# Performance work log

Hardware: AMD Instinct MI355X
Metric: run time of the kernel (lower is better)

## Reference

```python
import jax, jax.numpy as jnp
import numpy as np

B, S_NEW, D = 2, 1024, 2048
CACHE_LEN = 4096
H, KVH, HD = 32, 8, 64
REP = H // KVH  # 4
POS = 3072


def setup_inputs() -> dict:
    key = jax.random.key(0)
    ks = jax.random.split(key, 11)
    sc = 0.02
    return {
        "x": jax.random.normal(ks[0], (B, S_NEW, D), jnp.float32),
        "k_cache": jax.random.normal(ks[1], (B, CACHE_LEN, KVH, HD), jnp.float32),
        "v_cache": jax.random.normal(ks[2], (B, CACHE_LEN, KVH, HD), jnp.float32),
        "Wq": jax.random.normal(ks[3], (D, H * HD), jnp.float32) * sc,
        "bq": jax.random.normal(ks[4], (H * HD,), jnp.float32) * sc,
        "Wk": jax.random.normal(ks[5], (D, KVH * HD), jnp.float32) * sc,
        "bk": jax.random.normal(ks[6], (KVH * HD,), jnp.float32) * sc,
        "Wv": jax.random.normal(ks[7], (D, KVH * HD), jnp.float32) * sc,
        "bv": jax.random.normal(ks[8], (KVH * HD,), jnp.float32) * sc,
        "Wo": jax.random.normal(ks[9], (H * HD, D), jnp.float32) * sc,
        "bo": jax.random.normal(ks[10], (D,), jnp.float32) * sc,
        "input_pos": POS,
    }


def reference(x, k_cache, v_cache, Wq, bq, Wk, bk, Wv, bv, Wo, bo, input_pos):
    b, s, _ = x.shape
    # projections
    q = (x @ Wq + bq).reshape(b, s, H, HD)
    k = (x @ Wk + bk).reshape(b, s, KVH, HD)
    v = (x @ Wv + bv).reshape(b, s, KVH, HD)
    # KV-cache append (input_pos is a static Python int)
    k_cache = jax.lax.dynamic_update_slice(k_cache, k, (0, input_pos, 0, 0))
    v_cache = jax.lax.dynamic_update_slice(v_cache, v, (0, input_pos, 0, 0))
    T = input_pos + s
    ck = k_cache[:b, :T]  # [b, T, KVH, HD]
    cv = v_cache[:b, :T]
    # GQA: query head h attends with kv head h // REP -> group q as [b, KVH, REP, s, HD]
    qg = q.reshape(b, s, KVH, REP, HD)
    scale = 1.0 / np.sqrt(HD).astype(np.float32)
    # scores: [b, KVH, REP, s, T]
    scores = jnp.einsum("bsgrd,btgd->bgrst", qg, ck) * scale
    weights = jax.nn.softmax(scores, axis=-1)
    # out: [b, KVH, REP, s, HD] -> [b, s, H*HD]
    z = jnp.einsum("bgrst,btgd->bsgrd", weights, cv).reshape(b, s, H * HD)
    return z @ Wo + bo
```

## Files before the change

### kernel.cpp

```cpp
#include <hip/hip_runtime.h>

#define BB   2
#define SS   1024
#define DD   2048
#define CL   4096
#define HH   32
#define KVH  8
#define HD   64
#define POS  3072
#define TTOT 4096
#define NQKV 3072

typedef __bf16 bfv8 __attribute__((ext_vector_type(8)));
typedef __bf16 bfv4 __attribute__((ext_vector_type(4)));
typedef unsigned short usv8 __attribute__((ext_vector_type(8)));
typedef unsigned short usv4 __attribute__((ext_vector_type(4)));
typedef float f32x4 __attribute__((ext_vector_type(4)));

#define QSCALE 0.18033688011112042f

static __device__ __forceinline__ unsigned short f2bf(float f) {
  return __builtin_bit_cast(unsigned short, (__bf16)f);
}

static __device__ __forceinline__ float fexp2(float x) {
  float r;
  asm("v_exp_f32 %0, %1" : "=v"(r) : "v"(x));
  return r;
}

static __device__ __forceinline__ f32x4 mfma16(bfv8 a, bfv8 b, f32x4 c) {
  return __builtin_amdgcn_mfma_f32_16x16x32_bf16(a, b, c, 0, 0, 0);
}

static __device__ __forceinline__ void gload16(const unsigned short* g, unsigned short* l) {
  typedef const __attribute__((address_space(1))) unsigned int GU;
  typedef __attribute__((address_space(3))) unsigned int LU;
  __builtin_amdgcn_global_load_lds((GU*)(unsigned long long)(uintptr_t)g,
                                   (LU*)(unsigned int)(uintptr_t)l, 16, 0, 0);
}

#define WAIT_VM0_BARRIER() do { \
  asm volatile("s_waitcnt vmcnt(0)" : : : "memory"); \
  __builtin_amdgcn_s_barrier(); } while (0)

__global__ __launch_bounds__(256) void conv_x_kernel(
    const float* __restrict__ x, const float* __restrict__ bq,
    const float* __restrict__ bk, const float* __restrict__ bv,
    unsigned short* __restrict__ xb, float* __restrict__ biasws) {
  int gid = blockIdx.x * 256 + threadIdx.x;
  if (gid < NQKV)
    biasws[gid] = gid < 2048 ? bq[gid] : (gid < 2560 ? bk[gid - 2048] : bv[gid - 2560]);
  f32x4 v = reinterpret_cast<const f32x4*>(x)[gid];
  usv4 o;
#pragma unroll
  for (int e = 0; e < 4; ++e) o[e] = f2bf(v[e]);
  reinterpret_cast<usv4*>(xb)[gid] = o;
}

__global__ __launch_bounds__(256) void trw_kernel(const float* __restrict__ src, int Ns,
                                                  unsigned short* __restrict__ dst) {
  __shared__ unsigned short L[64][72];
  const int n0 = blockIdx.x * 64, k0 = blockIdx.y * 64;
  const int tid = threadIdx.x;
#pragma unroll
  for (int p = 0; p < 4; ++p) {
    int r = p * 16 + (tid >> 4), c4 = tid & 15;
    f32x4 v = *reinterpret_cast<const f32x4*>(src + (long)(k0 + r) * Ns + n0 + c4 * 4);
#pragma unroll
    for (int e = 0; e < 4; ++e) L[r][c4 * 4 + e] = f2bf(v[e]);
  }
  __syncthreads();
  int n = tid >> 2, kc = (tid & 3) * 16;
  usv8 a, b;
#pragma unroll
  for (int e = 0; e < 8; ++e) { a[e] = L[kc + e][n]; b[e] = L[kc + 8 + e][n]; }
  unsigned short* dp = dst + (long)(n0 + n) * DD + k0 + kc;
  *reinterpret_cast<usv8*>(dp) = a;
  *reinterpret_cast<usv8*>(dp + 8) = b;
}

__global__ __launch_bounds__(256) void kcopy_kernel(const float* __restrict__ kc,
                                                    unsigned short* __restrict__ Kb) {
  int i = blockIdx.x * 256 + threadIdx.x;
  const int PERB = POS * KVH * 16;
  int b = i / PERB, rem = i - b * PERB;
  int t = rem / (KVH * 16), r2 = rem - t * (KVH * 16);
  int g = r2 >> 4, d4 = r2 & 15;
  f32x4 v = reinterpret_cast<const f32x4*>(kc)[(((long)((b * CL + t) * KVH + g)) << 4) + d4];
  usv4 o;
#pragma unroll
  for (int e = 0; e < 4; ++e) o[e] = f2bf(v[e]);
  reinterpret_cast<usv4*>(Kb)[(((long)((b * KVH + g) * CL + t)) << 4) + d4] = o;
}

__global__ __launch_bounds__(256) void vtrans_kernel(const float* __restrict__ vc,
                                                     unsigned short* __restrict__ Vb) {
  __shared__ unsigned short L[64][72];
  const int t0 = (blockIdx.x % 48) * 64;
  const int g = (blockIdx.x / 48) % KVH;
  const int b = blockIdx.x / (48 * KVH);
  const int tid = threadIdx.x;
  const int r = tid >> 2;
#pragma unroll
  for (int p = 0; p < 4; ++p) {
    int f = (tid & 3) + p * 4;
    f32x4 v = reinterpret_cast<const f32x4*>(vc)[(((long)(b * CL + t0 + r) * KVH + g) << 4) + f];
#pragma unroll
    for (int e = 0; e < 4; ++e) L[r][f * 4 + e] = f2bf(v[e]);
  }
  __syncthreads();
  int d = tid >> 2, tc = (tid & 3) * 16;
  usv8 a, b8;
#pragma unroll
  for (int e = 0; e < 8; ++e) { a[e] = L[tc + e][d]; b8[e] = L[tc + 8 + e][d]; }
  unsigned short* dp = Vb + (((long)((b * KVH + g) * HD + d)) << 12) + t0 + tc;
  *reinterpret_cast<usv8*>(dp) = a;
  *reinterpret_cast<usv8*>(dp + 8) = b8;
}

template <int MODE>
__global__ __launch_bounds__(256) void gemm2_kernel(
    const unsigned short* __restrict__ A, const unsigned short* __restrict__ Bt,
    const float* __restrict__ bias, float* __restrict__ outp,
    unsigned short* __restrict__ qout, unsigned short* __restrict__ kout,
    unsigned short* __restrict__ vout, int N, int K) {
  __shared__ unsigned short Al[2][64 * 32];
  __shared__ unsigned short Bl[2][128 * 32];
  const int tid = threadIdx.x;
  const int lane = tid & 63, w = tid >> 6;
  const int lr = lane & 15, lg = lane >> 4;
  const int wr = (w & 1) * 32, wc = (w >> 1) * 64;
  const int m0 = blockIdx.y * 64, n0 = blockIdx.x * 128;
  f32x4 acc[2][4];
#pragma unroll
  for (int a = 0; a < 2; ++a)
#pragma unroll
    for (int c = 0; c < 4; ++c) acc[a][c] = (f32x4){0.f, 0.f, 0.f, 0.f};

  const unsigned short* ga = A + (long)(m0 + 16 * w + (lane >> 2)) * K + (lane & 3) * 8;
  const unsigned short* gb = Bt + (long)(n0 + 32 * w + (lane >> 2)) * K + (lane & 3) * 8;
  unsigned short* const Al0 = &Al[0][0];
  unsigned short* const Al1 = &Al[1][0];
  unsigned short* const Bl0 = &Bl[0][0];
  unsigned short* const Bl1 = &Bl[1][0];
  const int wa = w * 512, wb = w * 1024;

  gload16(ga,          Al0 + wa);
  gload16(gb,          Bl0 + wb);
  gload16(gb + 16 * K, Bl0 + wb + 512);

  const int NIT = K >> 5;
  for (int it = 0; it < NIT; ++it) {
    WAIT_VM0_BARRIER();
    const bool odd = it & 1;
    const unsigned short* Ard = odd ? Al1 : Al0;
    const unsigned short* Brd = odd ? Bl1 : Bl0;
    if (it + 1 < NIT) {
      int kn = (it + 1) * 32;
      unsigned short* ad = (odd ? Al0 : Al1) + wa;
      unsigned short* bd = (odd ? Bl0 : Bl1) + wb;
      gload16(ga + kn,          ad);
      gload16(gb + kn,          bd);
      gload16(gb + kn + 16 * K, bd + 512);
    }
    bfv8 af[2], bf_[4];
#pragma unroll
    for (int mi = 0; mi < 2; ++mi)
      af[mi] = *reinterpret_cast<const bfv8*>(Ard + (wr + mi * 16 + lr) * 32 + lg * 8);
#pragma unroll
    for (int ni = 0; ni < 4; ++ni)
      bf_[ni] = *reinterpret_cast<const bfv8*>(Brd + (wc + ni * 16 + lr) * 32 + lg * 8);
#pragma unroll
    for (int mi = 0; mi < 2; ++mi)
#pragma unroll
      for (int ni = 0; ni < 4; ++ni)
        acc[mi][ni] = mfma16(af[mi], bf_[ni], acc[mi][ni]);
    __builtin_amdgcn_s_barrier();
  }

#pragma unroll
  for (int mi = 0; mi < 2; ++mi) {
#pragma unroll
    for (int ni = 0; ni < 4; ++ni) {
      int gn = n0 + wc + ni * 16 + lr;
      float bvl = bias[gn];
      float vals[4];
#pragma unroll
      for (int j = 0; j < 4; ++j) vals[j] = acc[mi][ni][j] + bvl;
      int gmb = m0 + wr + mi * 16 + lg * 4;
      if constexpr (MODE == 1) {
#pragma unroll
        for (int j = 0; j < 4; ++j) outp[(long)(gmb + j) * N + gn] = vals[j];
      } else {
        int b = gmb >> 10, s = gmb & 1023;
        if (gn < 2048) {
          int h = gn >> 6, d = gn & 63;
#pragma unroll
          for (int j = 0; j < 4; ++j)
            qout[(((long)((b * HH + h) * SS + s + j)) << 6) + d] = f2bf(vals[j] * QSCALE);
        } else if (gn < 2560) {
          int g = (gn - 2048) >> 6, d = gn & 63;
#pragma unroll
          for (int j = 0; j < 4; ++j)
            kout[(((long)((b * KVH + g) * CL + POS + s + j)) << 6) + d] = f2bf(vals[j]);
        } else {
          int g = (gn - 2560) >> 6, d = gn & 63;
          usv4 o;
#pragma unroll
          for (int j = 0; j < 4; ++j) o[j] = f2bf(vals[j]);
          *reinterpret_cast<usv4*>(vout + (((long)((b * KVH + g) * HD + d)) << 12) + POS + s) = o;
        }
      }
    }
  }
}

__global__ __launch_bounds__(256) void attn_kernel(
    const unsigned short* __restrict__ Q, const unsigned short* __restrict__ Kb,
    const unsigned short* __restrict__ Vb, unsigned short* __restrict__ Z) {
  __shared__ unsigned short Kl[2 * 64 * 64];
  __shared__ unsigned short Vl[2 * 64 * 64];
  __shared__ unsigned short Pl[4 * 16 * 64];

  const int tid = threadIdx.x;
  const int lane = tid & 63, w = tid >> 6;
  const int lr = lane & 15, lg = lane >> 4;
  const int s0 = blockIdx.x * 64;
  const int h = blockIdx.y, b = blockIdx.z, g = h >> 2;
  const int sw = s0 + w * 16;
  const int woff = w * 1024;

  const unsigned short* qb = Q + (((long)((b * HH + h) * SS + sw + lr)) << 6) + lg * 8;
  bfv8 qf0 = *reinterpret_cast<const bfv8*>(qb);
  bfv8 qf1 = *reinterpret_cast<const bfv8*>(qb + 32);

  const unsigned short* kg = Kb + (((long)(b * KVH + g)) << 18);
  const unsigned short* vg = Vb + (((long)(b * KVH + g)) << 18);

  const int rw = lane >> 3;
  const int ug = (lane & 7) ^ rw;
  const unsigned short* kA = kg + (16 * w + rw) * 64 + ug * 8;
  const unsigned short* vA = vg + (long)(16 * w + rw) * TTOT + ug * 8;

  unsigned short* const Kl0 = Kl;
  unsigned short* const Kl1 = Kl + 4096;
  unsigned short* const Vl0 = Vl;
  unsigned short* const Vl1 = Vl + 4096;

  const int sz = lr & 7;
  const int u0 = (lg ^ sz) * 8, u1 = ((lg ^ sz) ^ 4) * 8;

  const int swzP = (lr & 7) << 3;
  unsigned short* const prow = Pl + (w * 16 + lr) * 64;
  const int p0 = (lg * 8) ^ swzP, p1 = (32 + lg * 8) ^ swzP;

  f32x4 O[4];
#pragma unroll
  for (int dt = 0; dt < 4; ++dt) O[dt] = (f32x4){0.f, 0.f, 0.f, 0.f};
  float lsum = 0.f;

  gload16(kA,            Kl0 + woff);
  gload16(kA + 8 * 64,   Kl0 + woff + 512);
  gload16(vA,            Vl0 + woff);
  gload16(vA + 8 * TTOT, Vl0 + woff + 512);

  for (int it = 0; it < 64; ++it) {
    WAIT_VM0_BARRIER();
    const bool odd = it & 1;
    const unsigned short* krd = odd ? Kl1 : Kl0;
    const unsigned short* vrd = odd ? Vl1 : Vl0;
    if (it < 63) {
      int tn = (it + 1) * 64;
      unsigned short* kwd = (odd ? Kl0 : Kl1) + woff;
      unsigned short* vwd = (odd ? Vl0 : Vl1) + woff;
      gload16(kA + tn * 64,           kwd);
      gload16(kA + tn * 64 + 8 * 64,  kwd + 512);
      gload16(vA + tn,                vwd);
      gload16(vA + tn + 8 * TTOT,     vwd + 512);
    }

    __builtin_amdgcn_s_setprio(1);
    f32x4 sv[4];
#pragma unroll
    for (int tt = 0; tt < 4; ++tt) {
      const unsigned short* kr = krd + (tt * 16 + lr) * 64;
      bfv8 kf0 = *reinterpret_cast<const bfv8*>(kr + u0);
      bfv8 kf1 = *reinterpret_cast<const bfv8*>(kr + u1);
      f32x4 z = (f32x4){0.f, 0.f, 0.f, 0.f};
      z = mfma16(kf0, qf0, z);
      z = mfma16(kf1, qf1, z);
      sv[tt] = z;
    }
    __builtin_amdgcn_s_setprio(0);

    float ps = 0.f;
#pragma unroll
    for (int tt = 0; tt < 4; ++tt)
#pragma unroll
      for (int j = 0; j < 4; ++j) {
        float p = fexp2(sv[tt][j]);
        sv[tt][j] = p;
        ps += p;
      }
    lsum += ps;

#pragma unroll
    for (int tt = 0; tt < 4; ++tt) {
      bfv4 pv;
#pragma unroll
      for (int j = 0; j < 4; ++j) pv[j] = (__bf16)sv[tt][j];
      *reinterpret_cast<bfv4*>(&prow[(tt * 16 + lg * 4) ^ swzP]) = pv;
    }

    bfv8 pf0 = *reinterpret_cast<const bfv8*>(&prow[p0]);
    bfv8 pf1 = *reinterpret_cast<const bfv8*>(&prow[p1]);
    __builtin_amdgcn_s_setprio(1);
#pragma unroll
    for (int dt = 0; dt < 4; ++dt) {
      const unsigned short* vr = vrd + (dt * 16 + lr) * 64;
      bfv8 vf0 = *reinterpret_cast<const bfv8*>(vr + u0);
      bfv8 vf1 = *reinterpret_cast<const bfv8*>(vr + u1);
      O[dt] = mfma16(pf0, vf0, O[dt]);
      O[dt] = mfma16(pf1, vf1, O[dt]);
    }
    __builtin_amdgcn_s_setprio(0);
    __builtin_amdgcn_s_barrier();
  }

  lsum += __shfl_xor(lsum, 16);
  lsum += __shfl_xor(lsum, 32);
  float lj[4];
#pragma unroll
  for (int j = 0; j < 4; ++j) lj[j] = 1.0f / __shfl(lsum, lg * 4 + j);
#pragma unroll
  for (int dt = 0; dt < 4; ++dt)
#pragma unroll
    for (int j = 0; j < 4; ++j) {
      int s = sw + lg * 4 + j, d = dt * 16 + lr;
      Z[(((long)(b * SS + s)) << 11) + h * 64 + d] = f2bf(O[dt][j] * lj[j]);
    }
}

extern "C" void kernel_launch(void* const* d_in, const int* in_sizes, int n_in,
                              void* d_out, int out_size, void* d_ws, size_t ws_size,
                              hipStream_t stream) {
  const float* x  = (const float*)d_in[0];
  const float* kc = (const float*)d_in[1];
  const float* vc = (const float*)d_in[2];
  const float* Wq = (const float*)d_in[3];
  const float* bq = (const float*)d_in[4];
  const float* Wk = (const float*)d_in[5];
  const float* bk = (const float*)d_in[6];
  const float* Wv = (const float*)d_in[7];
  const float* bv = (const float*)d_in[8];
  const float* Wo = (const float*)d_in[9];
  const float* bo = (const float*)d_in[10];

  unsigned short* Kb    = (unsigned short*)d_ws;
  unsigned short* Vb    = Kb + 4194304;
  unsigned short* q_ws  = Vb + 4194304;
  unsigned short* xb    = q_ws + 4194304;
  unsigned short* z_ws  = xb;
  unsigned short* Wqkvt = xb + 4194304;
  unsigned short* Wot   = Wqkvt + 6291456;
  float* biasws = (float*)(Wot + 4194304);

  conv_x_kernel<<<4096, 256, 0, stream>>>(x, bq, bk, bv, xb, biasws);
  trw_kernel<<<dim3(32, 32), 256, 0, stream>>>(Wq, 2048, Wqkvt);
  trw_kernel<<<dim3(8, 32), 256, 0, stream>>>(Wk, 512, Wqkvt + (long)2048 * 2048);
  trw_kernel<<<dim3(8, 32), 256, 0, stream>>>(Wv, 512, Wqkvt + (long)2560 * 2048);
  trw_kernel<<<dim3(32, 32), 256, 0, stream>>>(Wo, 2048, Wot);
  kcopy_kernel<<<3072, 256, 0, stream>>>(kc, Kb);
  vtrans_kernel<<<768, 256, 0, stream>>>(vc, Vb);
  gemm2_kernel<0><<<dim3(24, 32), 256, 0, stream>>>(xb, Wqkvt, biasws, nullptr,
                                                    q_ws, Kb, Vb, NQKV, DD);
  attn_kernel<<<dim3(16, 32, 2), 256, 0, stream>>>(q_ws, Kb, Vb, z_ws);
  gemm2_kernel<1><<<dim3(16, 32), 256, 0, stream>>>(z_ws, Wot, bo, (float*)d_out,
                                                    nullptr, nullptr, nullptr, DD, DD);
}
```

Baseline: 321.2 us.

## Merge prep kernels, drop redundant loop barriers, split attention PV into halves

The four weight-transpose launches become one kernel, and the K-copy and V-transpose launches become another, with branching on block index. This cuts the number of small prep-kernel launches. The GEMM and attention main loops drop their trailing s_barrier, relying on the wait-plus-barrier at the top of each iteration to protect the double buffers. The GEMM MFMA block is also wrapped in setprio. In attention, the per-wave P staging buffer is halved and the PV product runs in two phases, so the second half's bf16 conversion and stores can overlap the first half's MFMAs. The cost is extra LDS round trips on a buffer that is reused within each iteration.

```diff
diff --git a/kernel.cpp b/kernel.cpp
--- a/kernel.cpp
+++ b/kernel.cpp
@@ -58,10 +58,19 @@
   reinterpret_cast<usv4*>(xb)[gid] = o;
 }
 
-__global__ __launch_bounds__(256) void trw_kernel(const float* __restrict__ src, int Ns,
-                                                  unsigned short* __restrict__ dst) {
+__global__ __launch_bounds__(256) void wtr_kernel(
+    const float* __restrict__ Wq, const float* __restrict__ Wk,
+    const float* __restrict__ Wv, const float* __restrict__ Wo,
+    unsigned short* __restrict__ Wqkvt, unsigned short* __restrict__ Wot) {
   __shared__ unsigned short L[64][72];
-  const int n0 = blockIdx.x * 64, k0 = blockIdx.y * 64;
+  const int bx = blockIdx.x, k0 = blockIdx.y * 64;
+  const float* src;
+  unsigned short* dst;
+  int Ns, n0;
+  if (bx < 32)      { src = Wq; Ns = 2048; dst = Wqkvt;                     n0 = bx * 64; }
+  else if (bx < 40) { src = Wk; Ns = 512;  dst = Wqkvt + (long)2048 * 2048; n0 = (bx - 32) * 64; }
+  else if (bx < 48) { src = Wv; Ns = 512;  dst = Wqkvt + (long)2560 * 2048; n0 = (bx - 40) * 64; }
+  else              { src = Wo; Ns = 2048; dst = Wot;                       n0 = (bx - 48) * 64; }
   const int tid = threadIdx.x;
 #pragma unroll
   for (int p = 0; p < 4; ++p) {
@@ -80,43 +89,44 @@
   *reinterpret_cast<usv8*>(dp + 8) = b;
 }
 
-__global__ __launch_bounds__(256) void kcopy_kernel(const float* __restrict__ kc,
-                                                    unsigned short* __restrict__ Kb) {
-  int i = blockIdx.x * 256 + threadIdx.x;
-  const int PERB = POS * KVH * 16;
-  int b = i / PERB, rem = i - b * PERB;
-  int t = rem / (KVH * 16), r2 = rem - t * (KVH * 16);
-  int g = r2 >> 4, d4 = r2 & 15;
-  f32x4 v = reinterpret_cast<const f32x4*>(kc)[(((long)((b * CL + t) * KVH + g)) << 4) + d4];
-  usv4 o;
-#pragma unroll
-  for (int e = 0; e < 4; ++e) o[e] = f2bf(v[e]);
-  reinterpret_cast<usv4*>(Kb)[(((long)((b * KVH + g) * CL + t)) << 4) + d4] = o;
-}
-
-__global__ __launch_bounds__(256) void vtrans_kernel(const float* __restrict__ vc,
-                                                     unsigned short* __restrict__ Vb) {
-  __shared__ unsigned short L[64][72];
-  const int t0 = (blockIdx.x % 48) * 64;
-  const int g = (blockIdx.x / 48) % KVH;
-  const int b = blockIdx.x / (48 * KVH);
+__global__ __launch_bounds__(256) void cache_kernel(
+    const float* __restrict__ kc, const float* __restrict__ vc,
+    unsigned short* __restrict__ Kb, unsigned short* __restrict__ Vb) {
   const int tid = threadIdx.x;
-  const int r = tid >> 2;
-#pragma unroll
-  for (int p = 0; p < 4; ++p) {
-    int f = (tid & 3) + p * 4;
-    f32x4 v = reinterpret_cast<const f32x4*>(vc)[(((long)(b * CL + t0 + r) * KVH + g) << 4) + f];
-#pragma unroll
-    for (int e = 0; e < 4; ++e) L[r][f * 4 + e] = f2bf(v[e]);
+  if (blockIdx.x < 3072) {
+    int i = blockIdx.x * 256 + tid;
+    const int PERB = POS * KVH * 16;
+    int b = i / PERB, rem = i - b * PERB;
+    int t = rem / (KVH * 16), r2 = rem - t * (KVH * 16);
+    int g = r2 >> 4, d4 = r2 & 15;
+    f32x4 v = reinterpret_cast<const f32x4*>(kc)[(((long)((b * CL + t) * KVH + g)) << 4) + d4];
+    usv4 o;
+#pragma unroll
+    for (int e = 0; e < 4; ++e) o[e] = f2bf(v[e]);
+    reinterpret_cast<usv4*>(Kb)[(((long)((b * KVH + g) * CL + t)) << 4) + d4] = o;
+  } else {
+    __shared__ unsigned short L[64][72];
+    const int bid = blockIdx.x - 3072;
+    const int t0 = (bid % 48) * 64;
+    const int g = (bid / 48) % KVH;
+    const int b = bid / (48 * KVH);
+    const int r = tid >> 2;
+#pragma unroll
+    for (int p = 0; p < 4; ++p) {
+      int f = (tid & 3) + p * 4;
+      f32x4 v = reinterpret_cast<const f32x4*>(vc)[(((long)(b * CL + t0 + r) * KVH + g) << 4) + f];
+#pragma unroll
+      for (int e = 0; e < 4; ++e) L[r][f * 4 + e] = f2bf(v[e]);
+    }
+    __syncthreads();
+    int d = tid >> 2, tc = (tid & 3) * 16;
+    usv8 a, b8;
+#pragma unroll
+    for (int e = 0; e < 8; ++e) { a[e] = L[tc + e][d]; b8[e] = L[tc + 8 + e][d]; }
+    unsigned short* dp = Vb + (((long)((b * KVH + g) * HD + d)) << 12) + t0 + tc;
+    *reinterpret_cast<usv8*>(dp) = a;
+    *reinterpret_cast<usv8*>(dp + 8) = b8;
   }
-  __syncthreads();
-  int d = tid >> 2, tc = (tid & 3) * 16;
-  usv8 a, b8;
-#pragma unroll
-  for (int e = 0; e < 8; ++e) { a[e] = L[tc + e][d]; b8[e] = L[tc + 8 + e][d]; }
-  unsigned short* dp = Vb + (((long)((b * KVH + g) * HD + d)) << 12) + t0 + tc;
-  *reinterpret_cast<usv8*>(dp) = a;
-  *reinterpret_cast<usv8*>(dp + 8) = b8;
 }
 
 template <int MODE>
@@ -171,12 +181,13 @@
 #pragma unroll
     for (int ni = 0; ni < 4; ++ni)
       bf_[ni] = *reinterpret_cast<const bfv8*>(Brd + (wc + ni * 16 + lr) * 32 + lg * 8);
+    __builtin_amdgcn_s_setprio(1);
 #pragma unroll
     for (int mi = 0; mi < 2; ++mi)
 #pragma unroll
       for (int ni = 0; ni < 4; ++ni)
         acc[mi][ni] = mfma16(af[mi], bf_[ni], acc[mi][ni]);
-    __builtin_amdgcn_s_barrier();
+    __builtin_amdgcn_s_setprio(0);
   }
 
 #pragma unroll
@@ -221,7 +232,7 @@
     const unsigned short* __restrict__ Vb, unsigned short* __restrict__ Z) {
   __shared__ unsigned short Kl[2 * 64 * 64];
   __shared__ unsigned short Vl[2 * 64 * 64];
-  __shared__ unsigned short Pl[4 * 16 * 64];
+  __shared__ unsigned short Pl[4 * 16 * 32];
 
   const int tid = threadIdx.x;
   const int lane = tid & 63, w = tid >> 6;
@@ -251,9 +262,9 @@
   const int sz = lr & 7;
   const int u0 = (lg ^ sz) * 8, u1 = ((lg ^ sz) ^ 4) * 8;
 
-  const int swzP = (lr & 7) << 3;
-  unsigned short* const prow = Pl + (w * 16 + lr) * 64;
-  const int p0 = (lg * 8) ^ swzP, p1 = (32 + lg * 8) ^ swzP;
+  const int swzP = (lr & 3) << 3;
+  unsigned short* const prow = Pl + (w * 16 + lr) * 32;
+  const int p0 = (lg * 8) ^ swzP;
 
   f32x4 O[4];
 #pragma unroll
@@ -306,26 +317,38 @@
     lsum += ps;
 
 #pragma unroll
-    for (int tt = 0; tt < 4; ++tt) {
+    for (int tt = 0; tt < 2; ++tt) {
       bfv4 pv;
 #pragma unroll
       for (int j = 0; j < 4; ++j) pv[j] = (__bf16)sv[tt][j];
       *reinterpret_cast<bfv4*>(&prow[(tt * 16 + lg * 4) ^ swzP]) = pv;
     }
-
     bfv8 pf0 = *reinterpret_cast<const bfv8*>(&prow[p0]);
-    bfv8 pf1 = *reinterpret_cast<const bfv8*>(&prow[p1]);
     __builtin_amdgcn_s_setprio(1);
 #pragma unroll
     for (int dt = 0; dt < 4; ++dt) {
       const unsigned short* vr = vrd + (dt * 16 + lr) * 64;
       bfv8 vf0 = *reinterpret_cast<const bfv8*>(vr + u0);
+      O[dt] = mfma16(pf0, vf0, O[dt]);
+    }
+    __builtin_amdgcn_s_setprio(0);
+
+#pragma unroll
+    for (int tt = 2; tt < 4; ++tt) {
+      bfv4 pv;
+#pragma unroll
+      for (int j = 0; j < 4; ++j) pv[j] = (__bf16)sv[tt][j];
+      *reinterpret_cast<bfv4*>(&prow[((tt - 2) * 16 + lg * 4) ^ swzP]) = pv;
+    }
+    bfv8 pf1 = *reinterpret_cast<const bfv8*>(&prow[p0]);
+    __builtin_amdgcn_s_setprio(1);
+#pragma unroll
+    for (int dt = 0; dt < 4; ++dt) {
+      const unsigned short* vr = vrd + (dt * 16 + lr) * 64;
       bfv8 vf1 = *reinterpret_cast<const bfv8*>(vr + u1);
-      O[dt] = mfma16(pf0, vf0, O[dt]);
       O[dt] = mfma16(pf1, vf1, O[dt]);
     }
     __builtin_amdgcn_s_setprio(0);
-    __builtin_amdgcn_s_barrier();
   }
 
   lsum += __shfl_xor(lsum, 16);
@@ -367,12 +390,8 @@
   float* biasws = (float*)(Wot + 4194304);
 
   conv_x_kernel<<<4096, 256, 0, stream>>>(x, bq, bk, bv, xb, biasws);
-  trw_kernel<<<dim3(32, 32), 256, 0, stream>>>(Wq, 2048, Wqkvt);
-  trw_kernel<<<dim3(8, 32), 256, 0, stream>>>(Wk, 512, Wqkvt + (long)2048 * 2048);
-  trw_kernel<<<dim3(8, 32), 256, 0, stream>>>(Wv, 512, Wqkvt + (long)2560 * 2048);
-  trw_kernel<<<dim3(32, 32), 256, 0, stream>>>(Wo, 2048, Wot);
-  kcopy_kernel<<<3072, 256, 0, stream>>>(kc, Kb);
-  vtrans_kernel<<<768, 256, 0, stream>>>(vc, Vb);
+  wtr_kernel<<<dim3(80, 32), 256, 0, stream>>>(Wq, Wk, Wv, Wo, Wqkvt, Wot);
+  cache_kernel<<<3840, 256, 0, stream>>>(kc, vc, Kb, Vb);
   gemm2_kernel<0><<<dim3(24, 32), 256, 0, stream>>>(xb, Wqkvt, biasws, nullptr,
                                                     q_ws, Kb, Vb, NQKV, DD);
   attn_kernel<<<dim3(16, 32, 2), 256, 0, stream>>>(q_ws, Kb, Vb, z_ws);
```

Result: slower. 329.7 us (+2.6%).
